# Kernel tuning notes

Hardware: AMD Instinct MI355X
Metric: run time of the kernel (lower is better)

The kernel has to match this reference:

```python
import jax, jax.numpy as jnp
import numpy as np

LN_EPS = 1e-5

def _layer_norm(x, gamma, beta):
    m = jnp.mean(x, axis=-1, keepdims=True)
    v = jnp.mean((x - m) ** 2, axis=-1, keepdims=True)
    return (x - m) / jnp.sqrt(v + LN_EPS) * gamma + beta

def setup_inputs() -> dict:
    key = jax.random.key(0)
    k1, k2, k3 = jax.random.split(key, 3)
    N, E, D = 8192, 4096, 128
    node_embeddings = jax.random.normal(k1, (N, D), dtype=jnp.float32)
    target_matrix = jax.random.normal(k2, (N, N), dtype=jnp.float32)
    hypergraph_matrix = jax.random.randint(k3, (N, E), 0, 2, dtype=jnp.int32)
    ln_gamma = jnp.ones((D,), dtype=jnp.float32)
    ln_beta = jnp.zeros((D,), dtype=jnp.float32)
    return {
        "node_embeddings": node_embeddings,
        "target_matrix": target_matrix,
        "ln_gamma": ln_gamma,
        "ln_beta": ln_beta,
        "hypergraph_matrix": hypergraph_matrix,
        "num_layers": 3,
    }

def reference(node_embeddings, target_matrix, ln_gamma, ln_beta, hypergraph_matrix, num_layers):
    x = node_embeddings  # [N, D]
    for _ in range(num_layers):
        t = jnp.matmul(target_matrix, x)        # [N, D]
        x = jnp.matmul(target_matrix.T, t)      # [N, D]
        x = _layer_norm(x, ln_gamma, ln_beta)
        # dropout is identity in eval mode
    # per-hyperedge masked mean over nodes, vectorized as a dense GEMV-style reduce
    h = (hypergraph_matrix > 0).astype(x.dtype)            # [N, E]
    counts = jnp.sum(h, axis=0)                            # [E]
    sums = jnp.einsum('ne,nd->ed', h, x)                   # [E, D]
    means = sums / counts[:, None]                         # [E, D]
    return jnp.max(means, axis=0)                          # [D]
```

## Files before the change

### kernel.cpp

```cpp
#include <hip/hip_runtime.h>
#include <cstdint>
#include <cstddef>

typedef __attribute__((ext_vector_type(8))) short short8;
typedef __attribute__((ext_vector_type(4))) short short4v;
typedef __attribute__((ext_vector_type(4))) float float4v;
typedef __attribute__((ext_vector_type(4))) int int4v;
typedef unsigned short ushort_t;

__device__ __forceinline__ ushort_t f2bf(float f) {
  unsigned u = __builtin_bit_cast(unsigned, f);
  u = (u + 0x7FFFu + ((u >> 16) & 1u)) >> 16;
  return (ushort_t)u;
}
__device__ __forceinline__ float bf2f(ushort_t h) {
  unsigned u = ((unsigned)h) << 16;
  return __builtin_bit_cast(float, u);
}

__device__ __forceinline__ void gld_lds16(const void* g, void* l) {
  __builtin_amdgcn_global_load_lds(
      (const __attribute__((address_space(1))) void*)g,
      (__attribute__((address_space(3))) void*)l, 16, 0, 0);
}

__global__ __launch_bounds__(256, 3) void gemm_tn(
    const ushort_t* __restrict__ A, const ushort_t* __restrict__ B,
    float* __restrict__ P, int M, int N, int K) {
  __shared__ ushort_t As[128 * 64];
  __shared__ ushort_t Bs[128 * 64];
  const int tid = threadIdx.x;
  const int lane = tid & 63;
  const int wave = tid >> 6;
  const int wm = (wave & 1) * 64;
  const int wn = (wave >> 1) * 64;
  const int m0 = blockIdx.x * 128;
  const int n0 = blockIdx.y * 128;
  int t0, tl;
  if (blockIdx.z < 8) { t0 = blockIdx.z * 11; tl = 11; }
  else { t0 = 88 + (blockIdx.z - 8) * 10; tl = 10; }
  float* __restrict__ Pc = P + (size_t)blockIdx.z * M * N;

  float4v acc[4][4] = {};

  for (int t = t0; t < t0 + tl; t++) {
    const ushort_t* Ag = A + (size_t)m0 * K + t * 64;
    const ushort_t* Bg = B + (size_t)n0 * K + t * 64;
#pragma unroll
    for (int i = 0; i < 4; i++) {
      int f = i * 4096 + tid * 16;
      int r = f >> 7;
      int cb = f & 127;
      gld_lds16((const char*)(Ag + (size_t)r * K) + cb, (char*)As + f);
      gld_lds16((const char*)(Bg + (size_t)r * K) + cb, (char*)Bs + f);
    }
    __syncthreads();
#pragma unroll
    for (int ks = 0; ks < 64; ks += 32) {
      short8 af[4], bfr[4];
      const int kr = ks + (lane >> 4) * 8;
      const int l15 = lane & 15;
#pragma unroll
      for (int im = 0; im < 4; im++)
        af[im] = *(const short8*)&As[(wm + im * 16 + l15) * 64 + kr];
#pragma unroll
      for (int in = 0; in < 4; in++)
        bfr[in] = *(const short8*)&Bs[(wn + in * 16 + l15) * 64 + kr];
#pragma unroll
      for (int im = 0; im < 4; im++)
#pragma unroll
        for (int in = 0; in < 4; in++)
          acc[im][in] = __builtin_amdgcn_mfma_f32_16x16x32_bf16(
              af[im], bfr[in], acc[im][in], 0, 0, 0);
    }
    __syncthreads();
  }
  const int cn = lane & 15;
  const int cr = (lane >> 4) * 4;
#pragma unroll
  for (int im = 0; im < 4; im++)
#pragma unroll
    for (int in = 0; in < 4; in++)
#pragma unroll
      for (int r = 0; r < 4; r++) {
        int m = wm + im * 16 + cr + r;
        int n = wn + in * 16 + cn;
        Pc[(size_t)(m0 + m) * N + (n0 + n)] = acc[im][in][r];
      }
}

__global__ __launch_bounds__(256) void dualcast_f32_k(
    const float* __restrict__ src, ushort_t* __restrict__ dstN,
    ushort_t* __restrict__ dstT, int R, int C) {
  __shared__ float tile[64][65];
  const int c0 = blockIdx.x * 64, r0 = blockIdx.y * 64;
  const int tr = threadIdx.x >> 2, cs = (threadIdx.x & 3) * 16;
  const float* s = src + (size_t)(r0 + tr) * C + c0 + cs;
  float v[16];
#pragma unroll
  for (int j = 0; j < 16; j += 4) {
    float4v t4 = *(const float4v*)(s + j);
    v[j] = t4.x; v[j + 1] = t4.y; v[j + 2] = t4.z; v[j + 3] = t4.w;
  }
  if (dstN) {
    ushort_t o[16];
#pragma unroll
    for (int j = 0; j < 16; j++) o[j] = f2bf(v[j]);
    ushort_t* d = dstN + (size_t)(r0 + tr) * C + c0 + cs;
    *(short8*)d = *(const short8*)&o[0];
    *(short8*)(d + 8) = *(const short8*)&o[8];
  }
#pragma unroll
  for (int j = 0; j < 16; j++) tile[tr][cs + j] = v[j];
  __syncthreads();
  const int tc = threadIdx.x >> 2, rs = (threadIdx.x & 3) * 16;
  ushort_t o[16];
#pragma unroll
  for (int j = 0; j < 16; j++) o[j] = f2bf(tile[rs + j][tc]);
  ushort_t* d = dstT + (size_t)(c0 + tc) * R + r0 + rs;
  *(short8*)d = *(const short8*)&o[0];
  *(short8*)(d + 8) = *(const short8*)&o[8];
}

__global__ __launch_bounds__(256) void tcast_i32_k(
    const int* __restrict__ src, ushort_t* __restrict__ dstT, int R, int C) {
  __shared__ float tile[64][65];
  const int c0 = blockIdx.x * 64, r0 = blockIdx.y * 64;
  const int tr = threadIdx.x >> 2, cs = (threadIdx.x & 3) * 16;
  const int* s = src + (size_t)(r0 + tr) * C + c0 + cs;
#pragma unroll
  for (int j = 0; j < 16; j += 4) {
    int4v t4 = *(const int4v*)(s + j);
    tile[tr][cs + j] = t4.x > 0 ? 1.f : 0.f;
    tile[tr][cs + j + 1] = t4.y > 0 ? 1.f : 0.f;
    tile[tr][cs + j + 2] = t4.z > 0 ? 1.f : 0.f;
    tile[tr][cs + j + 3] = t4.w > 0 ? 1.f : 0.f;
  }
  __syncthreads();
  const int tc = threadIdx.x >> 2, rs = (threadIdx.x & 3) * 16;
  ushort_t o[16];
#pragma unroll
  for (int j = 0; j < 16; j++) o[j] = f2bf(tile[rs + j][tc]);
  ushort_t* d = dstT + (size_t)(c0 + tc) * R + r0 + rs;
  *(short8*)d = *(const short8*)&o[0];
  *(short8*)(d + 8) = *(const short8*)&o[8];
}

__global__ __launch_bounds__(256) void counts_k(
    const ushort_t* __restrict__ hT, float* __restrict__ counts, int Nn) {
  const int e = blockIdx.x * 4 + (threadIdx.x >> 6);
  const int lane = threadIdx.x & 63;
  const ushort_t* row = hT + (size_t)e * Nn;
  float s = 0.f;
  for (int i = 0; i < Nn / 512; i++) {
    short8 v = *(const short8*)&row[i * 512 + lane * 8];
#pragma unroll
    for (int j = 0; j < 8; j++) s += bf2f(((ushort_t*)&v)[j]);
  }
#pragma unroll
  for (int off = 32; off > 0; off >>= 1) s += __shfl_down(s, off);
  if (lane == 0) counts[e] = s;
}

__global__ __launch_bounds__(256) void cast_k(
    const float* __restrict__ P, ushort_t* __restrict__ out, int MN) {
  const int i = (blockIdx.x * 256 + threadIdx.x) * 8;
  float4v a = {0.f, 0.f, 0.f, 0.f}, b = {0.f, 0.f, 0.f, 0.f};
  for (int sp = 0; sp < 12; sp++) {
    a += *(const float4v*)&P[(size_t)sp * MN + i];
    b += *(const float4v*)&P[(size_t)sp * MN + i + 4];
  }
  ushort_t o[8];
  o[0] = f2bf(a.x); o[1] = f2bf(a.y); o[2] = f2bf(a.z); o[3] = f2bf(a.w);
  o[4] = f2bf(b.x); o[5] = f2bf(b.y); o[6] = f2bf(b.z); o[7] = f2bf(b.w);
  *(short8*)&out[i] = *(const short8*)o;
}

__global__ __launch_bounds__(256) void ln_cast_k(
    const float* __restrict__ P, const float* __restrict__ gamma,
    const float* __restrict__ beta, ushort_t* __restrict__ xT, int Ncols) {
  __shared__ float ssum[8][32], ssq[8][32];
  const int c = threadIdx.x & 31;
  const int q = threadIdx.x >> 5;
  const int m = blockIdx.x * 32 + c;
  const size_t DN = (size_t)128 * Ncols;
  float vloc[16];
  float s = 0.f, sq = 0.f;
#pragma unroll
  for (int j = 0; j < 16; j++) {
    const int d = q * 16 + j;
    float v = 0.f;
    for (int sp = 0; sp < 12; sp++)
      v += P[(size_t)sp * DN + (size_t)d * Ncols + m];
    vloc[j] = v; s += v; sq += v * v;
  }
  ssum[q][c] = s;
  ssq[q][c] = sq;
  __syncthreads();
  float S = 0.f, SQ = 0.f;
#pragma unroll
  for (int r = 0; r < 8; r++) { S += ssum[r][c]; SQ += ssq[r][c]; }
  const float mean = S * (1.f / 128.f);
  const float var = SQ * (1.f / 128.f) - mean * mean;
  const float inv = rsqrtf(var + 1e-5f);
#pragma unroll
  for (int j = 0; j < 16; j++) {
    const int d = q * 16 + j;
    xT[(size_t)d * Ncols + m] = f2bf((vloc[j] - mean) * inv * gamma[d] + beta[d]);
  }
}

__global__ __launch_bounds__(256) void mm1_k(
    const float* __restrict__ P, const float* __restrict__ counts,
    float* __restrict__ pm, int EMN) {
  __shared__ float4v red[8][32];
  const int el = threadIdx.x >> 5;
  const int l32 = threadIdx.x & 31;
  const int e0 = blockIdx.x * 16;
  float4v vmax = {-3.4e38f, -3.4e38f, -3.4e38f, -3.4e38f};
  for (int ee = el; ee < 16; ee += 8) {
    const int e = e0 + ee;
    float4v s = {0.f, 0.f, 0.f, 0.f};
    for (int sp = 0; sp < 12; sp++)
      s += *(const float4v*)&P[(size_t)sp * EMN + (size_t)e * 128 + l32 * 4];
    const float inv = 1.f / counts[e];
    s *= inv;
    vmax.x = fmaxf(vmax.x, s.x); vmax.y = fmaxf(vmax.y, s.y);
    vmax.z = fmaxf(vmax.z, s.z); vmax.w = fmaxf(vmax.w, s.w);
  }
  red[el][l32] = vmax;
  __syncthreads();
  if (el == 0) {
    float4v m = red[0][l32];
#pragma unroll
    for (int r = 1; r < 8; r++) {
      float4v t = red[r][l32];
      m.x = fmaxf(m.x, t.x); m.y = fmaxf(m.y, t.y);
      m.z = fmaxf(m.z, t.z); m.w = fmaxf(m.w, t.w);
    }
    *(float4v*)&pm[(size_t)blockIdx.x * 128 + l32 * 4] = m;
  }
}

__global__ __launch_bounds__(128) void mm2_k(
    const float* __restrict__ pm, float* __restrict__ out, int B) {
  const int d = threadIdx.x;
  float v = -3.4e38f;
  for (int b = 0; b < B; b++) v = fmaxf(v, pm[b * 128 + d]);
  out[d] = v;
}

extern "C" void kernel_launch(void* const* d_in, const int* in_sizes, int n_in,
                              void* d_out, int out_size, void* d_ws,
                              size_t ws_size, hipStream_t stream) {
  const float* x0 = (const float*)d_in[0];
  const float* T = (const float*)d_in[1];
  const float* gamma = (const float*)d_in[2];
  const float* beta = (const float*)d_in[3];
  const int* h = (const int*)d_in[4];
  float* out = (float*)d_out;

  const int N = 8192, E = 4096, D = 128, K = 8192, S = 12;

  char* ws = (char*)d_ws;
  size_t off = 0;
  auto alloc = [&](size_t bytes) {
    char* p = ws + off;
    off += (bytes + 255) & ~(size_t)255;
    return p;
  };
  ushort_t* Tb = (ushort_t*)alloc((size_t)N * N * 2);
  ushort_t* Tt = (ushort_t*)alloc((size_t)N * N * 2);
  ushort_t* hT = (ushort_t*)alloc((size_t)E * N * 2);
  ushort_t* xT = (ushort_t*)alloc((size_t)D * N * 2);
  ushort_t* tT = (ushort_t*)alloc((size_t)D * N * 2);
  float* P = (float*)alloc((size_t)S * D * N * 4);
  float* counts = (float*)alloc((size_t)E * 4);
  float* pm = (float*)alloc((size_t)256 * D * 4);
  (void)ws_size;

  dualcast_f32_k<<<dim3(N / 64, N / 64), 256, 0, stream>>>(T, Tb, Tt, N, N);
  dualcast_f32_k<<<dim3(D / 64, N / 64), 256, 0, stream>>>(x0, nullptr, xT, N, D);
  tcast_i32_k<<<dim3(E / 64, N / 64), 256, 0, stream>>>(h, hT, N, E);
  counts_k<<<E / 4, 256, 0, stream>>>(hT, counts, N);

  for (int layer = 0; layer < 3; layer++) {
    gemm_tn<<<dim3(1, N / 128, S), 256, 0, stream>>>(xT, Tb, P, D, N, K);
    cast_k<<<D * N / (256 * 8), 256, 0, stream>>>(P, tT, D * N);
    gemm_tn<<<dim3(1, N / 128, S), 256, 0, stream>>>(tT, Tt, P, D, N, K);
    ln_cast_k<<<N / 32, 256, 0, stream>>>(P, gamma, beta, xT, N);
  }
  gemm_tn<<<dim3(E / 128, 1, S), 256, 0, stream>>>(hT, xT, P, E, D, K);
  mm1_k<<<E / 16, 256, 0, stream>>>(P, counts, pm, E * D);
  mm2_k<<<1, 128, 0, stream>>>(pm, out, E / 16);
}
```

Baseline: 958.2 us.

## Drop transposed target copy using transpose-read NN GEMM and fuse hyperedge counts

Adds a gemm_nn kernel that reads the row-major bf16 target matrix directly, using LDS transpose reads (ds_read_b64_tr_b16), so the second GEMM in each layer no longer needs a separately transposed copy. The full N×N transpose-cast becomes a plain streaming cast, which saves one 128MB bf16 write and the workspace it occupied. Hyperedge counts are now computed as per-tile column partial sums inside the mask transpose kernel and reduced by a small kernel, so the bf16 mask is not reread. The risks are in the NN kernel: the B-tile swizzle and the inline asm transpose reads could cause LDS bank conflicts or be less efficient than the existing TN path.

```diff
diff --git a/kernel.cpp b/kernel.cpp
--- a/kernel.cpp
+++ b/kernel.cpp
@@ -89,6 +89,107 @@
       }
 }
 
+__global__ __launch_bounds__(256, 3) void gemm_nn(
+    const ushort_t* __restrict__ A, const ushort_t* __restrict__ B,
+    float* __restrict__ P, int M, int N, int K) {
+  __shared__ ushort_t As[128 * 64];
+  __shared__ ushort_t Bs[64 * 128];
+  const int tid = threadIdx.x;
+  const int lane = tid & 63;
+  const int wave = tid >> 6;
+  const int wm = (wave & 1) * 64;
+  const int wn = (wave >> 1) * 64;
+  const int m0 = blockIdx.x * 128;
+  const int n0 = blockIdx.y * 128;
+  int t0, tl;
+  if (blockIdx.z < 8) { t0 = blockIdx.z * 11; tl = 11; }
+  else { t0 = 88 + (blockIdx.z - 8) * 10; tl = 10; }
+  float* __restrict__ Pc = P + (size_t)blockIdx.z * M * N;
+
+  int brow[4], bcol[4];
+#pragma unroll
+  for (int i = 0; i < 4; i++) {
+    const int c = i * 256 + tid;
+    brow[i] = ((c >> 6) << 2) | ((c >> 1) & 3);
+    bcol[i] = (((c >> 3) & 7) << 4) | ((c & 1) << 3);
+  }
+  const int l15 = lane & 15;
+  const int hi = lane >> 4;
+  const unsigned BsB =
+      (unsigned)(uintptr_t)(__attribute__((address_space(3))) void*)Bs;
+  const unsigned trb = BsB + (unsigned)(hi * 2048) + (unsigned)(l15 * 8);
+
+  float4v acc[4][4] = {};
+
+  for (int t = t0; t < t0 + tl; t++) {
+    const ushort_t* Ag = A + (size_t)m0 * K + t * 64;
+    const ushort_t* Bg = B + (size_t)(t * 64) * N + n0;
+#pragma unroll
+    for (int i = 0; i < 4; i++) {
+      int f = i * 4096 + tid * 16;
+      int r = f >> 7;
+      int cb = f & 127;
+      gld_lds16((const char*)(Ag + (size_t)r * K) + cb, (char*)As + f);
+      gld_lds16((const char*)(Bg + (size_t)brow[i] * N + bcol[i]),
+                (char*)Bs + f);
+    }
+    __syncthreads();
+#pragma unroll
+    for (int ks = 0; ks < 64; ks += 32) {
+      short8 af[4];
+      const int kr = ks + hi * 8;
+#pragma unroll
+      for (int im = 0; im < 4; im++)
+        af[im] = *(const short8*)&As[(wm + im * 16 + l15) * 64 + kr];
+      short4v r0[4], r1[4];
+      const unsigned tb = trb + (unsigned)((ks >> 2) * 1024) + (unsigned)(wn * 8);
+#pragma unroll
+      for (int in = 0; in < 4; in++) {
+        asm volatile(
+            "ds_read_b64_tr_b16 %0, %2\n\t"
+            "ds_read_b64_tr_b16 %1, %2 offset:1024"
+            : "=&v"(r0[in]), "=&v"(r1[in])
+            : "v"(tb + (unsigned)(in * 128)));
+      }
+      asm volatile("s_waitcnt lgkmcnt(0)" ::: "memory");
+      __builtin_amdgcn_sched_barrier(0);
+#pragma unroll
+      for (int im = 0; im < 4; im++)
+#pragma unroll
+        for (int in = 0; in < 4; in++) {
+          short8 bf8 = __builtin_shufflevector(r0[in], r1[in],
+                                               0, 1, 2, 3, 4, 5, 6, 7);
+          acc[im][in] = __builtin_amdgcn_mfma_f32_16x16x32_bf16(
+              af[im], bf8, acc[im][in], 0, 0, 0);
+        }
+    }
+    __syncthreads();
+  }
+  const int cn = lane & 15;
+  const int cr = (lane >> 4) * 4;
+#pragma unroll
+  for (int im = 0; im < 4; im++)
+#pragma unroll
+    for (int in = 0; in < 4; in++)
+#pragma unroll
+      for (int r = 0; r < 4; r++) {
+        int m = wm + im * 16 + cr + r;
+        int n = wn + in * 16 + cn;
+        Pc[(size_t)(m0 + m) * N + (n0 + n)] = acc[im][in][r];
+      }
+}
+
+__global__ __launch_bounds__(256) void cast32_k(
+    const float* __restrict__ src, ushort_t* __restrict__ dst) {
+  const size_t i = ((size_t)blockIdx.x * 256 + threadIdx.x) * 8;
+  float4v a = *(const float4v*)(src + i);
+  float4v b = *(const float4v*)(src + i + 4);
+  ushort_t o[8];
+  o[0] = f2bf(a.x); o[1] = f2bf(a.y); o[2] = f2bf(a.z); o[3] = f2bf(a.w);
+  o[4] = f2bf(b.x); o[5] = f2bf(b.y); o[6] = f2bf(b.z); o[7] = f2bf(b.w);
+  *(short8*)&dst[i] = *(const short8*)o;
+}
+
 __global__ __launch_bounds__(256) void dualcast_f32_k(
     const float* __restrict__ src, ushort_t* __restrict__ dstN,
     ushort_t* __restrict__ dstT, int R, int C) {
@@ -123,7 +224,8 @@
 }
 
 __global__ __launch_bounds__(256) void tcast_i32_k(
-    const int* __restrict__ src, ushort_t* __restrict__ dstT, int R, int C) {
+    const int* __restrict__ src, ushort_t* __restrict__ dstT,
+    float* __restrict__ partial, int R, int C) {
   __shared__ float tile[64][65];
   const int c0 = blockIdx.x * 64, r0 = blockIdx.y * 64;
   const int tr = threadIdx.x >> 2, cs = (threadIdx.x & 3) * 16;
@@ -144,22 +246,20 @@
   ushort_t* d = dstT + (size_t)(c0 + tc) * R + r0 + rs;
   *(short8*)d = *(const short8*)&o[0];
   *(short8*)(d + 8) = *(const short8*)&o[8];
-}
-
-__global__ __launch_bounds__(256) void counts_k(
-    const ushort_t* __restrict__ hT, float* __restrict__ counts, int Nn) {
-  const int e = blockIdx.x * 4 + (threadIdx.x >> 6);
-  const int lane = threadIdx.x & 63;
-  const ushort_t* row = hT + (size_t)e * Nn;
+  if (threadIdx.x < 64) {
+    float sum = 0.f;
+#pragma unroll
+    for (int r = 0; r < 64; r++) sum += tile[r][threadIdx.x];
+    partial[(size_t)(r0 >> 6) * C + c0 + threadIdx.x] = sum;
+  }
+}
+
+__global__ __launch_bounds__(256) void counts2_k(
+    const float* __restrict__ partial, float* __restrict__ counts, int E) {
+  const int e = blockIdx.x * 256 + threadIdx.x;
   float s = 0.f;
-  for (int i = 0; i < Nn / 512; i++) {
-    short8 v = *(const short8*)&row[i * 512 + lane * 8];
-#pragma unroll
-    for (int j = 0; j < 8; j++) s += bf2f(((ushort_t*)&v)[j]);
-  }
-#pragma unroll
-  for (int off = 32; off > 0; off >>= 1) s += __shfl_down(s, off);
-  if (lane == 0) counts[e] = s;
+  for (int r = 0; r < 128; r++) s += partial[(size_t)r * E + e];
+  counts[e] = s;
 }
 
 __global__ __launch_bounds__(256) void cast_k(
@@ -270,24 +370,24 @@
     return p;
   };
   ushort_t* Tb = (ushort_t*)alloc((size_t)N * N * 2);
-  ushort_t* Tt = (ushort_t*)alloc((size_t)N * N * 2);
   ushort_t* hT = (ushort_t*)alloc((size_t)E * N * 2);
   ushort_t* xT = (ushort_t*)alloc((size_t)D * N * 2);
   ushort_t* tT = (ushort_t*)alloc((size_t)D * N * 2);
   float* P = (float*)alloc((size_t)S * D * N * 4);
   float* counts = (float*)alloc((size_t)E * 4);
+  float* partial = (float*)alloc((size_t)(N / 64) * E * 4);
   float* pm = (float*)alloc((size_t)256 * D * 4);
   (void)ws_size;
 
-  dualcast_f32_k<<<dim3(N / 64, N / 64), 256, 0, stream>>>(T, Tb, Tt, N, N);
+  cast32_k<<<(int)((size_t)N * N / 2048), 256, 0, stream>>>(T, Tb);
   dualcast_f32_k<<<dim3(D / 64, N / 64), 256, 0, stream>>>(x0, nullptr, xT, N, D);
-  tcast_i32_k<<<dim3(E / 64, N / 64), 256, 0, stream>>>(h, hT, N, E);
-  counts_k<<<E / 4, 256, 0, stream>>>(hT, counts, N);
+  tcast_i32_k<<<dim3(E / 64, N / 64), 256, 0, stream>>>(h, hT, partial, N, E);
+  counts2_k<<<E / 256, 256, 0, stream>>>(partial, counts, E);
 
   for (int layer = 0; layer < 3; layer++) {
     gemm_tn<<<dim3(1, N / 128, S), 256, 0, stream>>>(xT, Tb, P, D, N, K);
     cast_k<<<D * N / (256 * 8), 256, 0, stream>>>(P, tT, D * N);
-    gemm_tn<<<dim3(1, N / 128, S), 256, 0, stream>>>(tT, Tt, P, D, N, K);
+    gemm_nn<<<dim3(1, N / 128, S), 256, 0, stream>>>(tT, Tb, P, D, N, K);
     ln_cast_k<<<N / 32, 256, 0, stream>>>(P, gamma, beta, xT, N);
   }
   gemm_tn<<<dim3(E / 128, 1, S), 256, 0, stream>>>(hT, xT, P, E, D, K);
```

Result: faster. 829.0 us (-13.5%).
